# Optimization experiments

Hardware: AMD Instinct MI355X
Metric: run time of the kernel (lower is better)

Reference implementation:

```python
import jax, jax.numpy as jnp
import numpy as np

HEADS = 64
EMBED = 1024
PER_DIM = EMBED // HEADS  # 16
C, T, T_Y = 32, 1024, 1024
OUT_T = 1024  # must equal T_Y for the broadcasted matmul
SCALE = float(np.sqrt(EMBED))


def entmax15(x, axis=-1):
    """Exact alpha=1.5 entmax (Peters & Martins), sort-based threshold."""
    x = x - jnp.max(x, axis=axis, keepdims=True)
    x = x / 2.0
    xsrt = -jnp.sort(-x, axis=axis)  # descending
    d = x.shape[axis]
    shp = [1] * x.ndim
    shp[axis] = d
    rho = jnp.arange(1, d + 1, dtype=x.dtype).reshape(shp)
    mean = jnp.cumsum(xsrt, axis=axis) / rho
    mean_sq = jnp.cumsum(xsrt * xsrt, axis=axis) / rho
    ss = rho * (mean_sq - mean * mean)
    delta = jnp.clip((1.0 - ss) / rho, 0.0)
    tau = mean - jnp.sqrt(delta)
    support = jnp.sum((tau <= xsrt).astype(jnp.int32), axis=axis, keepdims=True)
    tau_star = jnp.take_along_axis(tau, support - 1, axis=axis)
    p = jnp.clip(x - tau_star, 0.0)
    return p * p


def setup_inputs() -> dict:
    key = jax.random.key(0)
    ks = jax.random.split(key, 10)
    return {
        "x_en": jax.random.normal(ks[0], (C, T, EMBED), jnp.float32),
        "y_de": jax.random.normal(ks[1], (C, T_Y, EMBED), jnp.float32),
        "wq": jax.random.normal(ks[2], (PER_DIM, PER_DIM), jnp.float32) * 0.25,
        "bq": jax.random.normal(ks[3], (PER_DIM,), jnp.float32) * 0.1,
        "wk": jax.random.normal(ks[4], (PER_DIM, PER_DIM), jnp.float32) * 0.25,
        "bk": jax.random.normal(ks[5], (PER_DIM,), jnp.float32) * 0.1,
        "wv": jax.random.normal(ks[6], (PER_DIM, PER_DIM), jnp.float32) * 0.25,
        "bv": jax.random.normal(ks[7], (PER_DIM,), jnp.float32) * 0.1,
        "conv_w": jax.random.normal(ks[8], (OUT_T, T), jnp.float32) * 0.03,
        "conv_b": jax.random.normal(ks[9], (OUT_T,), jnp.float32) * 0.1,
    }


def reference(x_en, y_de, wq, bq, wk, bk, wv, bv, conv_w, conv_b):
    c, t, e = x_en.shape
    t_y = y_de.shape[1]
    x = x_en.reshape(c, t, HEADS, PER_DIM)
    # Conv2d(T, OUT_T, kernel=1): 1x1 conv over the T-as-channels axis
    x = jnp.einsum('cthd,ot->cohd', x, conv_w) + conv_b[None, :, None, None]
    y = y_de.reshape(c, t_y, HEADS, PER_DIM)
    q = y @ wq.T + bq          # (C, T_y,  H, D)
    k = x @ wk.T + bk          # (C, OUT_T, H, D)
    v = x @ wv.T + bv          # (C, OUT_T, H, D)
    # matmul(q, k.transpose(2,3)) with batch dims (C, T_y) == (C, OUT_T)
    scores = jnp.matmul(q, jnp.swapaxes(k, 2, 3)) / SCALE  # (C, T_y, H, H)
    attn = entmax15(scores, axis=-1)
    out = jnp.matmul(attn, v)  # (C, T_y, H, D)
    return out.reshape(c, t_y, HEADS * PER_DIM)
```

## Files before the change

kernel.cpp:

```cpp
#include <hip/hip_runtime.h>


typedef __attribute__((ext_vector_type(8))) _Float16 f16x8;
typedef __attribute__((ext_vector_type(4))) _Float16 f16x4;
typedef __attribute__((ext_vector_type(2))) _Float16 f16x2;
typedef __attribute__((ext_vector_type(4))) float f32x4;

union pk4 { f16x2 h2[2]; f16x4 h4; };

__device__ __forceinline__ f16x2 pkrtz(float a, float b){
  return __builtin_bit_cast(f16x2, __builtin_amdgcn_cvt_pkrtz(a, b));
}

__device__ __forceinline__ void gl_lds16(const void* g, void* l){
  __builtin_amdgcn_global_load_lds((const __attribute__((address_space(1))) void*)g,
                                   (__attribute__((address_space(3))) void*)l, 16, 0, 0);
}

__global__ __launch_bounds__(256) void k_cvt_w(const float* __restrict__ w,
                                               _Float16* __restrict__ wh){
  int i = (blockIdx.x * 256 + threadIdx.x) * 4;
  float4 v = *(const float4*)(w + i);
  f16x4 o = {(_Float16)v.x, (_Float16)v.y, (_Float16)v.z, (_Float16)v.w};
  *(f16x4*)(wh + i) = o;
}

__global__ __launch_bounds__(256) void k_transpose(const float* __restrict__ x,
                                                   _Float16* __restrict__ xT){
  __shared__ float tile[64][65];
  const int c  = blockIdx.z;
  const int t0 = blockIdx.y * 64;
  const int e0 = blockIdx.x * 64;
  const int tid = threadIdx.x;
  const int c4 = tid & 15;
  const int rb = tid >> 4;
  const float* src = x + ((size_t)c << 20) + (size_t)(t0 + rb) * 1024 + e0 + c4 * 4;
  #pragma unroll
  for (int p = 0; p < 4; ++p){
    float4 v = *(const float4*)(src + (size_t)p * 16 * 1024);
    tile[rb + p*16][c4*4+0] = v.x;
    tile[rb + p*16][c4*4+1] = v.y;
    tile[rb + p*16][c4*4+2] = v.z;
    tile[rb + p*16][c4*4+3] = v.w;
  }
  __syncthreads();
  _Float16* dst = xT + ((size_t)c << 20) + (size_t)(e0 + rb) * 1024 + t0 + c4 * 4;
  #pragma unroll
  for (int p = 0; p < 4; ++p){
    const int el = rb + p*16;
    f16x4 o = {(_Float16)tile[c4*4+0][el], (_Float16)tile[c4*4+1][el],
               (_Float16)tile[c4*4+2][el], (_Float16)tile[c4*4+3][el]};
    *(f16x4*)(dst + (size_t)p * 16 * 1024) = o;
  }
}

__global__ __launch_bounds__(256) void k_gemm(const _Float16* __restrict__ Aw,
                                              const _Float16* __restrict__ BxT,
                                              const float* __restrict__ bias,
                                              _Float16* __restrict__ X2){
  __shared__ _Float16 As[128*32];
  __shared__ _Float16 Bs[128*32];
  __shared__ float biass[128];
  const int tid  = threadIdx.x;
  const int c    = blockIdx.z;
  const int brow = blockIdx.y;
  const int bcol = blockIdx.x;
  const int lane = tid & 63;
  const int wave = tid >> 6;
  const int wr = wave >> 1, wc = wave & 1;
  const int fr = lane & 15, fq = lane >> 4;

  if (tid < 128) biass[tid] = bias[brow*128 + tid];

  const _Float16* Ab = Aw  + (size_t)(brow*128) * 1024;
  const _Float16* Bb = BxT + ((size_t)c << 20) + (size_t)(bcol*128) * 1024;
  const int srow = tid >> 2;
  const int skc  = tid & 3;

  f32x4 acc[4][4];
  #pragma unroll
  for (int m = 0; m < 4; ++m)
    #pragma unroll
    for (int n = 0; n < 4; ++n)
      acc[m][n] = (f32x4){0.f, 0.f, 0.f, 0.f};

  for (int kt = 0; kt < 1024; kt += 32){
    const _Float16* ga = Ab + (size_t)srow * 1024 + kt + skc*8;
    const _Float16* gb = Bb + (size_t)srow * 1024 + kt + skc*8;
    gl_lds16(ga,           &As[tid*8]);
    gl_lds16(ga + 64*1024, &As[2048 + tid*8]);
    gl_lds16(gb,           &Bs[tid*8]);
    gl_lds16(gb + 64*1024, &Bs[2048 + tid*8]);
    __syncthreads();
    f16x8 aF[4], bF[4];
    #pragma unroll
    for (int m = 0; m < 4; ++m)
      aF[m] = *(const f16x8*)&As[(wr*64 + m*16 + fr)*32 + fq*8];
    #pragma unroll
    for (int n = 0; n < 4; ++n)
      bF[n] = *(const f16x8*)&Bs[(wc*64 + n*16 + fr)*32 + fq*8];
    #pragma unroll
    for (int m = 0; m < 4; ++m)
      #pragma unroll
      for (int n = 0; n < 4; ++n)
        acc[m][n] = __builtin_amdgcn_mfma_f32_16x16x32_f16(aF[m], bF[n], acc[m][n], 0, 0, 0);
    __syncthreads();
  }

  _Float16* Cb = X2 + ((size_t)c << 20) + (size_t)(brow*128) * 1024 + bcol*128;
  #pragma unroll
  for (int m = 0; m < 4; ++m){
    #pragma unroll
    for (int n = 0; n < 4; ++n){
      #pragma unroll
      for (int r = 0; r < 4; ++r){
        const int orow = wr*64 + m*16 + fq*4 + r;
        const int ocol = wc*64 + n*16 + fr;
        Cb[(size_t)orow * 1024 + ocol] = (_Float16)(acc[m][n][r] + biass[orow]);
      }
    }
  }
}

__global__ __launch_bounds__(256) void k_attn(const float* __restrict__ y_de,
                                              const _Float16* __restrict__ X2,
                                              const float* __restrict__ wq, const float* __restrict__ bq,
                                              const float* __restrict__ wk, const float* __restrict__ bk,
                                              const float* __restrict__ wv, const float* __restrict__ bv,
                                              float* __restrict__ out){
  const int tid  = threadIdx.x;
  const int wave = tid >> 6, lane = tid & 63;
  const size_t pair = (size_t)blockIdx.x * 4 + wave;
  const int l15 = lane & 15;
  const int g   = lane >> 4;

  f16x4 wqA, wkA, wvB;
  {
    float4 a = *(const float4*)(wq + l15*16 + g*4);
    float4 b = *(const float4*)(wk + l15*16 + g*4);
    float4 c = *(const float4*)(wv + l15*16 + g*4);
    wqA = (f16x4){(_Float16)a.x, (_Float16)a.y, (_Float16)a.z, (_Float16)a.w};
    wkA = (f16x4){(_Float16)b.x, (_Float16)b.y, (_Float16)b.z, (_Float16)b.w};
    wvB = (f16x4){(_Float16)c.x, (_Float16)c.y, (_Float16)c.z, (_Float16)c.w};
  }
  const float4 bqv = *(const float4*)(bq + g*4);
  const float4 bkv = *(const float4*)(bk + g*4);
  const float  bvv = bv[l15];

  const _Float16* xp = X2 + (pair << 10);
  f16x4 xF[4];
  #pragma unroll
  for (int kt = 0; kt < 4; ++kt)
    xF[kt] = *(const f16x4*)(xp + (kt*16 + l15)*16 + g*4);

  f16x4 kF[4], vF[4];
  #pragma unroll
  for (int kt = 0; kt < 4; ++kt){
    f32x4 t = __builtin_amdgcn_mfma_f32_16x16x16f16(wkA, xF[kt], (f32x4){0.f,0.f,0.f,0.f}, 0, 0, 0);
    kF[kt] = (f16x4){(_Float16)(t[0]+bkv.x), (_Float16)(t[1]+bkv.y),
                     (_Float16)(t[2]+bkv.z), (_Float16)(t[3]+bkv.w)};
    f32x4 s = __builtin_amdgcn_mfma_f32_16x16x16f16(xF[kt], wvB, (f32x4){0.f,0.f,0.f,0.f}, 0, 0, 0);
    vF[kt] = (f16x4){(_Float16)(s[0]+bvv), (_Float16)(s[1]+bvv),
                     (_Float16)(s[2]+bvv), (_Float16)(s[3]+bvv)};
  }

  const float* yp = y_de + (pair << 10);
  float* op = out + (pair << 10);

  const f16x2 ones = {(_Float16)1.f, (_Float16)1.f};
  const f16x2 zz   = {(_Float16)0.f, (_Float16)0.f};

  #pragma unroll
  for (int qt = 0; qt < 4; ++qt){
    float4 yv = *(const float4*)(yp + (qt*16 + l15)*16 + g*4);
    f16x4 yF = {(_Float16)yv.x, (_Float16)yv.y, (_Float16)yv.z, (_Float16)yv.w};
    f32x4 q = __builtin_amdgcn_mfma_f32_16x16x16f16(wqA, yF, (f32x4){0.f,0.f,0.f,0.f}, 0, 0, 0);
    f16x4 qF = {(_Float16)((q[0]+bqv.x)*0.015625f), (_Float16)((q[1]+bqv.y)*0.015625f),
                (_Float16)((q[2]+bqv.z)*0.015625f), (_Float16)((q[3]+bqv.w)*0.015625f)};

    f16x2 u8[8];
    #pragma unroll
    for (int kt = 0; kt < 4; ++kt){
      f32x4 s = __builtin_amdgcn_mfma_f32_16x16x16f16(kF[kt], qF, (f32x4){0.f,0.f,0.f,0.f}, 0, 0, 0);
      u8[kt*2+0] = pkrtz(s[0], s[1]);
      u8[kt*2+1] = pkrtz(s[2], s[3]);
    }

    f16x2 m0 = __builtin_elementwise_max(u8[0], u8[1]);
    f16x2 m1 = __builtin_elementwise_max(u8[2], u8[3]);
    f16x2 m2 = __builtin_elementwise_max(u8[4], u8[5]);
    f16x2 m3 = __builtin_elementwise_max(u8[6], u8[7]);
    m0 = __builtin_elementwise_max(m0, m1);
    m2 = __builtin_elementwise_max(m2, m3);
    m0 = __builtin_elementwise_max(m0, m2);
    float mx = fmaxf((float)m0[0], (float)m0[1]);
    mx = fmaxf(mx, __shfl_xor(mx, 16));
    mx = fmaxf(mx, __shfl_xor(mx, 32));

    float S1 = 0.f, S2 = 0.f;
    #pragma unroll
    for (int i = 0; i < 8; ++i){
      S1 = __builtin_amdgcn_fdot2(u8[i], ones,  S1, false);
      S2 = __builtin_amdgcn_fdot2(u8[i], u8[i], S2, false);
    }
    S1 += __shfl_xor(S1, 16); S2 += __shfl_xor(S2, 16);
    S1 += __shfl_xor(S1, 32); S2 += __shfl_xor(S2, 32);
    const float mean = S1 * 0.015625f;
    const float ss   = S2 - S1 * mean;
    float delta = fmaxf((1.0f - ss) * 0.015625f, 0.0f);
    float tau = mean - sqrtf(delta);
    tau = fminf(tau, mx - 0.125f);
    tau = fmaxf(tau, mx - 1.0f);

    #pragma unroll
    for (int it = 0; it < 4; ++it){
      f16x2 tt = pkrtz(tau, tau);
      float T1 = 0.f, T2 = 0.f;
      #pragma unroll
      for (int i = 0; i < 8; ++i){
        f16x2 r = __builtin_elementwise_max(u8[i] - tt, zz);
        T1 = __builtin_amdgcn_fdot2(r, ones, T1, false);
        T2 = __builtin_amdgcn_fdot2(r, r,    T2, false);
      }
      T1 += __shfl_xor(T1, 16); T2 += __shfl_xor(T2, 16);
      T1 += __shfl_xor(T1, 32); T2 += __shfl_xor(T2, 32);
      tau += (T2 - 1.0f) * __builtin_amdgcn_rcpf(2.0f * T1);
    }

    const f16x2 tt = pkrtz(tau, tau);
    f32x4 o = (f32x4){0.f, 0.f, 0.f, 0.f};
    #pragma unroll
    for (int kt = 0; kt < 4; ++kt){
      f16x2 r0 = __builtin_elementwise_max(u8[kt*2+0] - tt, zz);
      f16x2 r1 = __builtin_elementwise_max(u8[kt*2+1] - tt, zz);
      pk4 pp; pp.h2[0] = r0 * r0; pp.h2[1] = r1 * r1;
      o = __builtin_amdgcn_mfma_f32_16x16x16f16(pp.h4, vF[kt], o, 0, 0, 0);
    }

    #pragma unroll
    for (int r = 0; r < 4; ++r)
      op[(qt*16 + g*4 + r)*16 + l15] = o[r];
  }
}

extern "C" void kernel_launch(void* const* d_in, const int* in_sizes, int n_in,
                              void* d_out, int out_size, void* d_ws, size_t ws_size,
                              hipStream_t stream) {
  (void)in_sizes; (void)n_in; (void)out_size; (void)ws_size;
  const float* x_en   = (const float*)d_in[0];
  const float* y_de   = (const float*)d_in[1];
  const float* wq     = (const float*)d_in[2];
  const float* bq     = (const float*)d_in[3];
  const float* wk     = (const float*)d_in[4];
  const float* bk     = (const float*)d_in[5];
  const float* wv     = (const float*)d_in[6];
  const float* bv     = (const float*)d_in[7];
  const float* conv_w = (const float*)d_in[8];
  const float* conv_b = (const float*)d_in[9];
  float* out = (float*)d_out;

  char* ws = (char*)d_ws;
  _Float16* xT = (_Float16*)ws;
  _Float16* X2 = (_Float16*)(ws + (size_t)67108864);
  _Float16* wH = (_Float16*)d_out;

  k_cvt_w    <<<dim3(1024),       dim3(256), 0, stream>>>(conv_w, wH);
  k_transpose<<<dim3(16, 16, 32), dim3(256), 0, stream>>>(x_en, xT);
  k_gemm     <<<dim3(8, 8, 32),   dim3(256), 0, stream>>>(wH, xT, conv_b, X2);
  k_attn     <<<dim3(8192),       dim3(256), 0, stream>>>(y_de, X2, wq, bq, wk, bk, wv, bv, out);
}
```

Measured before the change: 216.9 us.

## Rewrite conv GEMM with 256x256 tiles, double-buffered LDS and swizzle

```diff
diff --git a/kernel.cpp b/kernel.cpp
--- a/kernel.cpp
+++ b/kernel.cpp
@@ -16,6 +16,11 @@
   __builtin_amdgcn_global_load_lds((const __attribute__((address_space(1))) void*)g,
                                    (__attribute__((address_space(3))) void*)l, 16, 0, 0);
 }
+
+#define ASM_BARRIER()  asm volatile("s_barrier" ::: "memory")
+#define WAIT_LGKM0()   asm volatile("s_waitcnt lgkmcnt(0)" ::: "memory")
+#define WAIT_VM8()     asm volatile("s_waitcnt vmcnt(8)" ::: "memory")
+#define WAIT_VM0()     asm volatile("s_waitcnt vmcnt(0)" ::: "memory")
 
 __global__ __launch_bounds__(256) void k_cvt_w(const float* __restrict__ w,
                                                _Float16* __restrict__ wh){
@@ -54,72 +59,113 @@
   }
 }
 
-__global__ __launch_bounds__(256) void k_gemm(const _Float16* __restrict__ Aw,
-                                              const _Float16* __restrict__ BxT,
-                                              const float* __restrict__ bias,
-                                              _Float16* __restrict__ X2){
-  __shared__ _Float16 As[128*32];
-  __shared__ _Float16 Bs[128*32];
-  __shared__ float biass[128];
+__global__ __launch_bounds__(512, 2) void k_gemm(const _Float16* __restrict__ Aw,
+                                                 const _Float16* __restrict__ BxT,
+                                                 const float* __restrict__ bias,
+                                                 _Float16* __restrict__ X2){
+  __shared__ _Float16 smem[65536];
+  char* ldsbase = (char*)smem;
   const int tid  = threadIdx.x;
   const int c    = blockIdx.z;
   const int brow = blockIdx.y;
   const int bcol = blockIdx.x;
   const int lane = tid & 63;
   const int wave = tid >> 6;
-  const int wr = wave >> 1, wc = wave & 1;
+  const int wrow = wave >> 2;
+  const int wcol = wave & 3;
   const int fr = lane & 15, fq = lane >> 4;
-
-  if (tid < 128) biass[tid] = bias[brow*128 + tid];
-
-  const _Float16* Ab = Aw  + (size_t)(brow*128) * 1024;
-  const _Float16* Bb = BxT + ((size_t)c << 20) + (size_t)(bcol*128) * 1024;
-  const int srow = tid >> 2;
-  const int skc  = tid & 3;
-
-  f32x4 acc[4][4];
-  #pragma unroll
-  for (int m = 0; m < 4; ++m)
+  const int fq16 = fq * 16;
+  const int swz  = (fr & 7) << 4;
+
+  const char* Ab8 = (const char*)(Aw  + (size_t)(brow*256) * 1024);
+  const char* Bb8 = (const char*)(BxT + ((size_t)c << 20) + (size_t)(bcol*256) * 1024);
+
+  const int srow  = tid >> 3;
+  const int cphys = (tid & 7) * 16;
+
+#define STAGE(kt_, b_) do {                                                    \
+    _Pragma("unroll")                                                          \
+    for (int ci = 0; ci < 4; ++ci){                                            \
+      const int row_ = srow + ci*64;                                           \
+      const int cl_  = cphys ^ ((row_ & 7) << 4);     \
+      gl_lds16(Ab8 + (size_t)row_*2048 + (kt_)*128 + cl_,                      \
+               ldsbase + (b_)*65536 + tid*16 + ci*8192);                       \
+      gl_lds16(Bb8 + (size_t)row_*2048 + (kt_)*128 + cl_,                      \
+               ldsbase + (b_)*65536 + 32768 + tid*16 + ci*8192);               \
+    }                                                                          \
+  } while(0)
+
+  f32x4 acc[8][4];
+  #pragma unroll
+  for (int m = 0; m < 8; ++m)
     #pragma unroll
     for (int n = 0; n < 4; ++n)
       acc[m][n] = (f32x4){0.f, 0.f, 0.f, 0.f};
 
-  for (int kt = 0; kt < 1024; kt += 32){
-    const _Float16* ga = Ab + (size_t)srow * 1024 + kt + skc*8;
-    const _Float16* gb = Bb + (size_t)srow * 1024 + kt + skc*8;
-    gl_lds16(ga,           &As[tid*8]);
-    gl_lds16(ga + 64*1024, &As[2048 + tid*8]);
-    gl_lds16(gb,           &Bs[tid*8]);
-    gl_lds16(gb + 64*1024, &Bs[2048 + tid*8]);
-    __syncthreads();
-    f16x8 aF[4], bF[4];
-    #pragma unroll
-    for (int m = 0; m < 4; ++m)
-      aF[m] = *(const f16x8*)&As[(wr*64 + m*16 + fr)*32 + fq*8];
-    #pragma unroll
-    for (int n = 0; n < 4; ++n)
-      bF[n] = *(const f16x8*)&Bs[(wc*64 + n*16 + fr)*32 + fq*8];
-    #pragma unroll
-    for (int m = 0; m < 4; ++m)
+#define COMPUTE(b_) do {                                                       \
+    const char* pA_ = ldsbase + (b_)*65536;                                    \
+    const char* pB_ = pA_ + 32768;                                             \
+    _Pragma("unroll")                                                          \
+    for (int kk = 0; kk < 2; ++kk){                                            \
+      f16x8 aF[8], bF[4];                                                      \
+      _Pragma("unroll")                                                        \
+      for (int m = 0; m < 8; ++m)                                              \
+        aF[m] = *(const f16x8*)(pA_ + (wrow*128 + m*16 + fr)*128               \
+                                    + ((kk*64 + fq16) ^ swz));                 \
+      _Pragma("unroll")                                                        \
+      for (int n = 0; n < 4; ++n)                                              \
+        bF[n] = *(const f16x8*)(pB_ + (wcol*64 + n*16 + fr)*128                \
+                                    + ((kk*64 + fq16) ^ swz));                 \
+      __builtin_amdgcn_s_setprio(1);                                           \
+      _Pragma("unroll")                                                        \
+      for (int m = 0; m < 8; ++m)                                              \
+        _Pragma("unroll")                                                      \
+        for (int n = 0; n < 4; ++n)                                            \
+          acc[m][n] = __builtin_amdgcn_mfma_f32_16x16x32_f16(aF[m], bF[n],     \
+                                                             acc[m][n],0,0,0); \
+      __builtin_amdgcn_s_setprio(0);                                           \
+    }                                                                          \
+  } while(0)
+
+  STAGE(0, 0);
+  STAGE(1, 1);
+  WAIT_VM8();
+  ASM_BARRIER();
+
+  #pragma unroll 2
+  for (int kt = 0; kt < 16; ++kt){
+    const int b = kt & 1;
+    COMPUTE(b);
+    if (kt < 15){
+      WAIT_LGKM0();
+      ASM_BARRIER();
+      if (kt < 14){
+        STAGE(kt + 2, b);
+        WAIT_VM8();
+      } else {
+        WAIT_VM0();
+      }
+      ASM_BARRIER();
+    }
+  }
+
+  _Float16* Cb = X2 + ((size_t)c << 20) + (size_t)(brow*256) * 1024 + bcol*256;
+  const float* bb = bias + brow*256;
+  #pragma unroll
+  for (int m = 0; m < 8; ++m){
+    #pragma unroll
+    for (int r = 0; r < 4; ++r){
+      const int orow = wrow*128 + m*16 + fq*4 + r;
+      const float bv = bb[orow];
       #pragma unroll
-      for (int n = 0; n < 4; ++n)
-        acc[m][n] = __builtin_amdgcn_mfma_f32_16x16x32_f16(aF[m], bF[n], acc[m][n], 0, 0, 0);
-    __syncthreads();
-  }
-
-  _Float16* Cb = X2 + ((size_t)c << 20) + (size_t)(brow*128) * 1024 + bcol*128;
-  #pragma unroll
-  for (int m = 0; m < 4; ++m){
-    #pragma unroll
-    for (int n = 0; n < 4; ++n){
-      #pragma unroll
-      for (int r = 0; r < 4; ++r){
-        const int orow = wr*64 + m*16 + fq*4 + r;
-        const int ocol = wc*64 + n*16 + fr;
-        Cb[(size_t)orow * 1024 + ocol] = (_Float16)(acc[m][n][r] + biass[orow]);
+      for (int n = 0; n < 4; ++n){
+        const int ocol = wcol*64 + n*16 + fr;
+        Cb[(size_t)orow * 1024 + ocol] = (_Float16)(acc[m][n][r] + bv);
       }
     }
   }
+#undef STAGE
+#undef COMPUTE
 }
 
 __global__ __launch_bounds__(256) void k_attn(const float* __restrict__ y_de,
@@ -266,6 +312,6 @@
 
   k_cvt_w    <<<dim3(1024),       dim3(256), 0, stream>>>(conv_w, wH);
   k_transpose<<<dim3(16, 16, 32), dim3(256), 0, stream>>>(x_en, xT);
-  k_gemm     <<<dim3(8, 8, 32),   dim3(256), 0, stream>>>(wH, xT, conv_b, X2);
+  k_gemm     <<<dim3(4, 4, 32),   dim3(512), 0, stream>>>(wH, xT, conv_b, X2);
   k_attn     <<<dim3(8192),       dim3(256), 0, stream>>>(y_de, X2, wq, bq, wk, bk, wv, bv, out);
 }
```

Measured after the change: 201.0 us. 7.3% less time.
